# Optimization experiments

Hardware: AMD Instinct MI355X
Metric: run time of the kernel (lower is better)

Reference implementation:

```python
import jax, jax.numpy as jnp
import numpy as np

B = 128          # batch (number of ragged segments)
MAX_LEN = 197    # DeiT: 196 patches + CLS, upper bound on kept tokens
D = 768          # embed dim (DeiT-Base)
H = 12           # heads
HD = 64          # head dim
L = 6            # number of late ragged blocks
FF = 3072        # mlp hidden = 4*D
NC = 1000        # classes
EPS = 1e-6       # timm ViT LayerNorm eps


def setup_inputs() -> dict:
    # deterministic ragged lengths in [60, 197]; Total = 17078
    lens = 60 + (np.arange(B) * 137) % 138
    cu = np.concatenate([[0], np.cumsum(lens)]).astype(np.int32)
    total = int(cu[-1])
    ks = jax.random.split(jax.random.key(0), 8)
    n = lambda k, shp, s: jax.random.normal(k, shp, jnp.float32) * s
    return {
        "packed": n(ks[0], (total, D), 1.0),
        "cu_seqlens": jnp.asarray(cu),
        # stacked per-block params (jax convention: W is [in, out])
        "norm1_w": jnp.ones((L, D), jnp.float32),
        "norm1_b": jnp.zeros((L, D), jnp.float32),
        "qkv_w": n(ks[1], (L, D, 3 * D), 0.02),
        "qkv_b": jnp.zeros((L, 3 * D), jnp.float32),
        "proj_w": n(ks[2], (L, D, D), 0.02),
        "proj_b": jnp.zeros((L, D), jnp.float32),
        "norm2_w": jnp.ones((L, D), jnp.float32),
        "norm2_b": jnp.zeros((L, D), jnp.float32),
        "fc1_w": n(ks[3], (L, D, FF), 0.02),
        "fc1_b": jnp.zeros((L, FF), jnp.float32),
        "fc2_w": n(ks[4], (L, FF, D), 0.02),
        "fc2_b": jnp.zeros((L, D), jnp.float32),
        "backnorm_w": jnp.ones((D,), jnp.float32),
        "backnorm_b": jnp.zeros((D,), jnp.float32),
        "head_w": n(ks[5], (D, NC), 0.02),
        "head_b": jnp.zeros((NC,), jnp.float32),
    }


def _ln(x, w, b):
    mu = x.mean(-1, keepdims=True)
    var = ((x - mu) ** 2).mean(-1, keepdims=True)
    return (x - mu) * jax.lax.rsqrt(var + EPS) * w + b


def reference(packed, cu_seqlens, norm1_w, norm1_b, qkv_w, qkv_b, proj_w, proj_b,
              norm2_w, norm2_b, fc1_w, fc1_b, fc2_w, fc2_b,
              backnorm_w, backnorm_b, head_w, head_b):
    total = packed.shape[0]
    cu = cu_seqlens.astype(jnp.int32)
    b = cu.shape[0] - 1
    lens = cu[1:] - cu[:-1]                                   # [B]
    pos = jnp.arange(MAX_LEN, dtype=jnp.int32)
    idx = jnp.clip(cu[:-1, None] + pos[None, :], 0, total - 1)  # [B,S]
    valid = pos[None, :] < lens[:, None]                       # [B,S]
    # unpack ragged [Total,D] -> padded [B,S,D]; invalid slots zeroed
    x = packed[idx] * valid[..., None]
    kmask = valid[:, None, None, :]                            # [B,1,1,S] key mask
    scale = 1.0 / np.sqrt(HD)

    def block(x, p):
        n1w, n1b, qw, qb, pw, pb, n2w, n2b, f1w, f1b, f2w, f2b = p
        h = _ln(x, n1w, n1b)
        qkv = (h @ qw + qb).reshape(b, MAX_LEN, 3, H, HD)
        q, k, v = qkv[:, :, 0], qkv[:, :, 1], qkv[:, :, 2]
        sc = jnp.einsum('bqhd,bkhd->bhqk', q, k) * scale
        sc = jnp.where(kmask, sc, jnp.float32(-1e30))
        a = jax.nn.softmax(sc, axis=-1)
        o = jnp.einsum('bhqk,bkhd->bqhd', a, v).reshape(b, MAX_LEN, D)
        x = x + (o @ pw + pb)
        h2 = _ln(x, n2w, n2b)
        x = x + (jax.nn.gelu(h2 @ f1w + f1b, approximate=False) @ f2w + f2b)
        return x, None

    params = (norm1_w, norm1_b, qkv_w, qkv_b, proj_w, proj_b,
              norm2_w, norm2_b, fc1_w, fc1_b, fc2_w, fc2_b)
    x, _ = jax.lax.scan(block, x, params)
    # CLS token is the first token of each segment (packed[cu_seqlens[:-1]])
    cls = _ln(x[:, 0], backnorm_w, backnorm_b)
    return cls @ head_w + head_b
```

## Files before the change

kernel.cpp:

```cpp
#include <hip/hip_runtime.h>
#include <cstdint>
#include <cstddef>

typedef __bf16 bf16x8 __attribute__((ext_vector_type(8)));
typedef __bf16 bf16x4 __attribute__((ext_vector_type(4)));
typedef float  f32x4  __attribute__((ext_vector_type(4)));

#define M_TOT 17078
#define D_ 768
#define FF_ 3072
#define NC_ 1000
#define NL_ 6
#define PS 232

__device__ __forceinline__ void gload16(const __bf16* g, __bf16* s) {
    __builtin_amdgcn_global_load_lds(
        (const __attribute__((address_space(1))) unsigned int*)g,
        (__attribute__((address_space(3))) unsigned int*)s, 16, 0, 0);
}

__device__ __forceinline__ f32x4 mfma16(bf16x8 a, bf16x8 b, f32x4 c) {
    return __builtin_amdgcn_mfma_f32_16x16x32_bf16(a, b, c, 0, 0, 0);
}

__device__ __forceinline__ float fast_gelu(float v) {
    const float x = v * 0.70710678118654752440f;
    const float ax = fabsf(x);
    const float t = __builtin_amdgcn_rcpf(fmaf(0.3275911f, ax, 1.0f));
    float p = fmaf(1.061405429f, t, -1.453152027f);
    p = fmaf(p, t, 1.421413741f);
    p = fmaf(p, t, -0.284496736f);
    p = fmaf(p, t, 0.254829592f);
    const float e = __expf(-ax * ax);
    const float erf_ax = fmaf(-p * t, e, 1.0f);
    const float erf_x = copysignf(erf_ax, x);
    return 0.5f * v * (1.0f + erf_x);
}

__global__ __launch_bounds__(256)
void transpose_all_kernel(const float* __restrict__ qkvw, const float* __restrict__ projw,
                          const float* __restrict__ f1w, const float* __restrict__ f2w,
                          __bf16* __restrict__ qkvT, __bf16* __restrict__ projT,
                          __bf16* __restrict__ f1T, __bf16* __restrict__ f2T) {
    __shared__ float tile[32][33];
    int bid = blockIdx.x;
    const float* W; __bf16* WT; int N, local;
    if (bid < 1728)      { W = qkvw; WT = qkvT; N = 2304; local = bid; }
    else if (bid < 2304) { W = projw; WT = projT; N = 768; local = bid - 1728; }
    else if (bid < 4608) { W = f1w;  WT = f1T;  N = 3072; local = bid - 2304; }
    else                 { W = f2w;  WT = f2T;  N = 768;  local = bid - 4608; }
    const int nx = N >> 5;
    const int n0 = (local % nx) * 32, k0 = (local / nx) * 32;
    const int tc = threadIdx.x & 31, tr = threadIdx.x >> 5;
#pragma unroll
    for (int i = 0; i < 4; ++i)
        tile[tr + i * 8][tc] = W[(size_t)(k0 + tr + i * 8) * N + n0 + tc];
    __syncthreads();
    const int Kd = (bid < 4608) ? 768 : 3072;
#pragma unroll
    for (int i = 0; i < 4; ++i)
        WT[(size_t)(n0 + tr + i * 8) * Kd + k0 + tc] = (__bf16)tile[tc][tr + i * 8];
}

__global__ __launch_bounds__(256)
void transpose_head_kernel(const float* __restrict__ W, __bf16* __restrict__ WT) {
    __shared__ float tile[32][33];
    const int n0 = blockIdx.x * 32, k0 = blockIdx.y * 32;
    const int tc = threadIdx.x & 31, tr = threadIdx.x >> 5;
#pragma unroll
    for (int i = 0; i < 4; ++i) {
        const int n = n0 + tc;
        tile[tr + i * 8][tc] = (n < NC_) ? W[(size_t)(k0 + tr + i * 8) * NC_ + n] : 0.f;
    }
    __syncthreads();
#pragma unroll
    for (int i = 0; i < 4; ++i)
        WT[(size_t)(n0 + tr + i * 8) * 768 + k0 + tc] = (__bf16)tile[tc][tr + i * 8];
}

__global__ __launch_bounds__(256)
void ln_kernel(const float* __restrict__ X, const float* __restrict__ wgt,
               const float* __restrict__ bia, __bf16* __restrict__ out, int nrows) {
    const int wid = blockIdx.x * 4 + (threadIdx.x >> 6);
    if (wid >= nrows) return;
    const int l = threadIdx.x & 63;
    const float* xr = X + (size_t)wid * D_;
    f32x4 a[3];
#pragma unroll
    for (int i = 0; i < 3; ++i) a[i] = *(const f32x4*)(xr + i * 256 + l * 4);
    float s = 0.f, ss = 0.f;
#pragma unroll
    for (int i = 0; i < 3; ++i)
#pragma unroll
        for (int j = 0; j < 4; ++j) { float v = a[i][j]; s += v; ss += v * v; }
#pragma unroll
    for (int off = 32; off; off >>= 1) { s += __shfl_xor(s, off); ss += __shfl_xor(ss, off); }
    const float mean = s * (1.f / 768.f);
    const float var  = ss * (1.f / 768.f) - mean * mean;
    const float rstd = rsqrtf(var + 1e-6f);
#pragma unroll
    for (int i = 0; i < 3; ++i) {
        f32x4 wv = *(const f32x4*)(wgt + i * 256 + l * 4);
        f32x4 bv = *(const f32x4*)(bia + i * 256 + l * 4);
        bf16x4 ov;
#pragma unroll
        for (int j = 0; j < 4; ++j)
            ov[j] = (__bf16)((a[i][j] - mean) * rstd * wv[j] + bv[j]);
        *(bf16x4*)(out + (size_t)wid * D_ + i * 256 + l * 4) = ov;
    }
}

__global__ __launch_bounds__(256)
void cls_ln_kernel(const float* __restrict__ X, const int* __restrict__ cu,
                   const float* __restrict__ wgt, const float* __restrict__ bia,
                   __bf16* __restrict__ out) {
    const int wid = blockIdx.x * 4 + (threadIdx.x >> 6);
    const int l = threadIdx.x & 63;
    const float* xr = X + (size_t)cu[wid] * D_;
    f32x4 a[3];
#pragma unroll
    for (int i = 0; i < 3; ++i) a[i] = *(const f32x4*)(xr + i * 256 + l * 4);
    float s = 0.f, ss = 0.f;
#pragma unroll
    for (int i = 0; i < 3; ++i)
#pragma unroll
        for (int j = 0; j < 4; ++j) { float v = a[i][j]; s += v; ss += v * v; }
#pragma unroll
    for (int off = 32; off; off >>= 1) { s += __shfl_xor(s, off); ss += __shfl_xor(ss, off); }
    const float mean = s * (1.f / 768.f);
    const float var  = ss * (1.f / 768.f) - mean * mean;
    const float rstd = rsqrtf(var + 1e-6f);
#pragma unroll
    for (int i = 0; i < 3; ++i) {
        f32x4 wv = *(const f32x4*)(wgt + i * 256 + l * 4);
        f32x4 bv = *(const f32x4*)(bia + i * 256 + l * 4);
        bf16x4 ov;
#pragma unroll
        for (int j = 0; j < 4; ++j)
            ov[j] = (__bf16)((a[i][j] - mean) * rstd * wv[j] + bv[j]);
        *(bf16x4*)(out + (size_t)wid * D_ + i * 256 + l * 4) = ov;
    }
}

template <int EPI>
__global__ __launch_bounds__(256, 4)
void gemm_kernel(const __bf16* __restrict__ A, const __bf16* __restrict__ BT,
                 const float* __restrict__ bias, __bf16* __restrict__ Cb,
                 float* __restrict__ Cf, int K, int N, int Mc, int gx, int gy) {
    __shared__ __bf16 As[128 * 64];
    __shared__ __bf16 Bs[128 * 64];

    const int CC = 12;
    const int bid = blockIdx.x;
    const int per_chunk = gy * CC;
    const int chunk = bid / per_chunk;
    const int within = bid - chunk * per_chunk;
    const int ccw = min(CC, gx - chunk * CC);
    const int nb = gy * ccw;
    const int q = nb >> 3, r = nb & 7;
    const int xcd = within & 7, off = within >> 3;
    const int swz = (xcd < r) ? (xcd * (q + 1) + off) : (r * (q + 1) + (xcd - r) * q + off);
    const int by = swz / ccw;
    const int bx = chunk * CC + (swz - by * ccw);
    const int row0 = by * 128, col0 = bx * 128;

    const int t = threadIdx.x;
    const int l = t & 63, w = t >> 6;

    const int srow = t >> 3;
    const int scol = (((t & 7) ^ (srow & 7)) << 3);
    const __bf16* pa0 = A + (size_t)min(row0 +      srow, Mc - 1) * K + scol;
    const __bf16* pa1 = A + (size_t)min(row0 + 32 + srow, Mc - 1) * K + scol;
    const __bf16* pa2 = A + (size_t)min(row0 + 64 + srow, Mc - 1) * K + scol;
    const __bf16* pa3 = A + (size_t)min(row0 + 96 + srow, Mc - 1) * K + scol;
    const __bf16* pb0 = BT + (size_t)(col0 +      srow) * K + scol;
    const __bf16* pb1 = BT + (size_t)(col0 + 32 + srow) * K + scol;
    const __bf16* pb2 = BT + (size_t)(col0 + 64 + srow) * K + scol;
    const __bf16* pb3 = BT + (size_t)(col0 + 96 + srow) * K + scol;

    const int wr = (w >> 1) * 64, wc = (w & 1) * 64;
    const int fr = l & 15, fg = l >> 4;

    f32x4 acc[4][4];
#pragma unroll
    for (int i = 0; i < 4; ++i)
#pragma unroll
        for (int j = 0; j < 4; ++j) acc[i][j] = (f32x4){0.f, 0.f, 0.f, 0.f};

    for (int k0 = 0; k0 < K; k0 += 64) {
        __syncthreads();
        gload16(pa0 + k0, As + t * 8);
        gload16(pa1 + k0, As + 2048 + t * 8);
        gload16(pa2 + k0, As + 4096 + t * 8);
        gload16(pa3 + k0, As + 6144 + t * 8);
        gload16(pb0 + k0, Bs + t * 8);
        gload16(pb1 + k0, Bs + 2048 + t * 8);
        gload16(pb2 + k0, Bs + 4096 + t * 8);
        gload16(pb3 + k0, Bs + 6144 + t * 8);
        __syncthreads();
#pragma unroll
        for (int ks = 0; ks < 2; ++ks) {
            bf16x8 af[4], bfv[4];
#pragma unroll
            for (int i = 0; i < 4; ++i) {
                const int ar = wr + i * 16 + fr;
                const int br = wc + i * 16 + fr;
                af[i]  = *(const bf16x8*)(As + ar * 64 + (((ks * 4 + fg) ^ (ar & 7)) << 3));
                bfv[i] = *(const bf16x8*)(Bs + br * 64 + (((ks * 4 + fg) ^ (br & 7)) << 3));
            }
#pragma unroll
            for (int mi = 0; mi < 4; ++mi)
#pragma unroll
                for (int ni = 0; ni < 4; ++ni)
                    acc[mi][ni] = mfma16(af[mi], bfv[ni], acc[mi][ni]);
        }
    }

    if (EPI == 1) {
#pragma unroll
        for (int mi = 0; mi < 4; ++mi) {
#pragma unroll
            for (int ni = 0; ni < 4; ++ni) {
                const int nn = col0 + wc + ni * 16 + fr;
                const float bv = bias[nn];
#pragma unroll
                for (int v = 0; v < 4; ++v) {
                    const int mm = row0 + wr + mi * 16 + fg * 4 + v;
                    if (mm < Mc) {
                        float* p = Cf + (size_t)mm * N + nn;
                        *p = *p + acc[mi][ni][v] + bv;
                    }
                }
            }
        }
    } else {
        __syncthreads();
        __bf16* rs = As + w * 1024;
#pragma unroll
        for (int mi = 0; mi < 4; ++mi) {
#pragma unroll
            for (int ni = 0; ni < 4; ++ni) {
                const int nn = col0 + wc + ni * 16 + fr;
                const float bv = bias[nn];
#pragma unroll
                for (int v = 0; v < 4; ++v) {
                    const int row = fg * 4 + v;
                    float val = acc[mi][ni][v] + bv;
                    if (EPI == 2)
                        val = fast_gelu(val);
                    const int gsw = (ni * 2 + (fr >> 3)) ^ (row & 7);
                    rs[row * 64 + gsw * 8 + (fr & 7)] = (__bf16)val;
                }
            }
            asm volatile("s_waitcnt lgkmcnt(0)" ::: "memory");
#pragma unroll
            for (int half = 0; half < 2; ++half) {
                const int rr = (l >> 3) + half * 8;
                const int gg = (l & 7) ^ (rr & 7);
                bf16x8 vrow = *(const bf16x8*)(rs + rr * 64 + gg * 8);
                const int mm = row0 + wr + mi * 16 + rr;
                if (mm < Mc)
                    *(bf16x8*)(Cb + (size_t)mm * N + col0 + wc + (l & 7) * 8) = vrow;
            }
            asm volatile("s_waitcnt lgkmcnt(0)" ::: "memory");
        }
    }
}

__global__ __launch_bounds__(256)
void head_gemm_kernel(const __bf16* __restrict__ A, const __bf16* __restrict__ BT,
                      const float* __restrict__ bias, float* __restrict__ out) {
    __shared__ __bf16 As[128 * 32];
    __shared__ __bf16 Bs[128 * 32];
    const int t = threadIdx.x;
    const int l = t & 63, w = t >> 6;
    const int col0 = blockIdx.x * 128;
    const int sr = t >> 2, sc = (t & 3) * 8;
    const __bf16* a0 = A + (size_t)sr * 768 + sc;
    const __bf16* a1 = A + (size_t)(sr + 64) * 768 + sc;
    const __bf16* b0 = BT + (size_t)(col0 + sr) * 768 + sc;
    const __bf16* b1 = BT + (size_t)(col0 + sr + 64) * 768 + sc;
    __bf16* sa0 = As + t * 8;
    __bf16* sa1 = As + 2048 + t * 8;
    __bf16* sb0 = Bs + t * 8;
    __bf16* sb1 = Bs + 2048 + t * 8;
    const int wr = (w >> 1) * 64, wc = (w & 1) * 64;
    const int fr = l & 15, fg = l >> 4;

    f32x4 acc[4][4];
#pragma unroll
    for (int i = 0; i < 4; ++i)
#pragma unroll
        for (int j = 0; j < 4; ++j) acc[i][j] = (f32x4){0.f, 0.f, 0.f, 0.f};

    for (int k0 = 0; k0 < 768; k0 += 32) {
        __syncthreads();
        gload16(a0 + k0, sa0);
        gload16(a1 + k0, sa1);
        gload16(b0 + k0, sb0);
        gload16(b1 + k0, sb1);
        __syncthreads();
        bf16x8 af[4], bfv[4];
#pragma unroll
        for (int i = 0; i < 4; ++i) {
            af[i]  = *(const bf16x8*)(As + (wr + i * 16 + fr) * 32 + fg * 8);
            bfv[i] = *(const bf16x8*)(Bs + (wc + i * 16 + fr) * 32 + fg * 8);
        }
#pragma unroll
        for (int mi = 0; mi < 4; ++mi)
#pragma unroll
            for (int ni = 0; ni < 4; ++ni)
                acc[mi][ni] = mfma16(af[mi], bfv[ni], acc[mi][ni]);
    }

#pragma unroll
    for (int mi = 0; mi < 4; ++mi) {
#pragma unroll
        for (int ni = 0; ni < 4; ++ni) {
            const int nn = col0 + wc + ni * 16 + fr;
            if (nn < NC_) {
                const float bv = bias[nn];
#pragma unroll
                for (int v = 0; v < 4; ++v) {
                    const int mm = wr + mi * 16 + fg * 4 + v;
                    out[(size_t)mm * NC_ + nn] = acc[mi][ni][v] + bv;
                }
            }
        }
    }
}

__global__ __launch_bounds__(256)
void attn_kernel(const __bf16* __restrict__ qkv, __bf16* __restrict__ o,
                 const int* __restrict__ cu, int b0) {
    __shared__ __bf16 VT[64 * PS];
    __shared__ __bf16 P[4 * 16 * PS];
    const int b = b0 + blockIdx.x, h = blockIdx.y;
    const int r0   = cu[b0];
    const int rowb = cu[b] - r0;
    const int len  = cu[b + 1] - cu[b];
    const int t = threadIdx.x, w = t >> 6, l = t & 63;
    const int fr = l & 15, fg = l >> 4;
    const size_t base = (size_t)rowb * 2304 + h * 64;

    for (int c = t; c < 224 * 8; c += 256) {
        const int key = c >> 3, d0 = (c & 7) * 8;
        bf16x8 vv;
        if (key < len) {
            vv = *(const bf16x8*)(qkv + base + 1536 + (size_t)key * 2304 + d0);
        } else {
#pragma unroll
            for (int j = 0; j < 8; ++j) vv[j] = (__bf16)0.f;
        }
#pragma unroll
        for (int j = 0; j < 8; ++j) VT[(d0 + j) * PS + key] = vv[j];
    }
    __syncthreads();

    __bf16* Pw = P + w * 16 * PS;
    const int NQ = (len + 15) >> 4;

    for (int qt = w; qt < NQ; qt += 4) {
        const int qrow = qt * 16 + fr;
        const int qtok = qrow < len ? qrow : len - 1;
        const size_t qoff = base + (size_t)qtok * 2304 + fg * 8;
        bf16x8 qf0 = *(const bf16x8*)(qkv + qoff);
        bf16x8 qf1 = *(const bf16x8*)(qkv + qoff + 32);

        f32x4 s[14];
#pragma unroll
        for (int kt = 0; kt < 14; ++kt) {
            const int key = kt * 16 + fr;
            const int ktok = key < len ? key : len - 1;
            const size_t koff = base + 768 + (size_t)ktok * 2304 + fg * 8;
            f32x4 a = {0.f, 0.f, 0.f, 0.f};
            a = mfma16(qf0, *(const bf16x8*)(qkv + koff), a);
            a = mfma16(qf1, *(const bf16x8*)(qkv + koff + 32), a);
            s[kt] = a;
        }

#pragma unroll
        for (int v = 0; v < 4; ++v) {
            float m = -1e30f;
#pragma unroll
            for (int kt = 0; kt < 14; ++kt) {
                float sv = (kt * 16 + fr < len) ? s[kt][v] * 0.125f : -1e30f;
                s[kt][v] = sv;
                m = fmaxf(m, sv);
            }
            m = fmaxf(m, __shfl_xor(m, 1, 16));
            m = fmaxf(m, __shfl_xor(m, 2, 16));
            m = fmaxf(m, __shfl_xor(m, 4, 16));
            m = fmaxf(m, __shfl_xor(m, 8, 16));
            float sum = 0.f;
#pragma unroll
            for (int kt = 0; kt < 14; ++kt) {
                float p = __expf(s[kt][v] - m);
                s[kt][v] = p;
                sum += p;
            }
            sum += __shfl_xor(sum, 1, 16);
            sum += __shfl_xor(sum, 2, 16);
            sum += __shfl_xor(sum, 4, 16);
            sum += __shfl_xor(sum, 8, 16);
            const float inv = 1.f / sum;
#pragma unroll
            for (int kt = 0; kt < 14; ++kt)
                Pw[(fg * 4 + v) * PS + kt * 16 + fr] = (__bf16)(s[kt][v] * inv);
        }
        asm volatile("s_waitcnt lgkmcnt(0)" ::: "memory");

#pragma unroll
        for (int nt = 0; nt < 4; ++nt) {
            f32x4 oa = {0.f, 0.f, 0.f, 0.f};
#pragma unroll
            for (int ks = 0; ks < 7; ++ks) {
                bf16x8 pa = *(const bf16x8*)(Pw + fr * PS + ks * 32 + fg * 8);
                bf16x8 vb = *(const bf16x8*)(VT + (nt * 16 + fr) * PS + ks * 32 + fg * 8);
                oa = mfma16(pa, vb, oa);
            }
#pragma unroll
            for (int v = 0; v < 4; ++v) {
                const int q = qt * 16 + fg * 4 + v;
                if (q < len)
                    o[(size_t)(rowb + q) * D_ + h * 64 + nt * 16 + fr] = (__bf16)oa[v];
            }
        }
    }
}

extern "C" void kernel_launch(void* const* d_in, const int* in_sizes, int n_in,
                              void* d_out, int out_size, void* d_ws, size_t ws_size,
                              hipStream_t stream) {
    const float* packed = (const float*)d_in[0];
    const int*   cu     = (const int*)d_in[1];
    const float* n1w = (const float*)d_in[2];
    const float* n1b = (const float*)d_in[3];
    const float* qkvw = (const float*)d_in[4];
    const float* qkvb = (const float*)d_in[5];
    const float* projw = (const float*)d_in[6];
    const float* projb = (const float*)d_in[7];
    const float* n2w = (const float*)d_in[8];
    const float* n2b = (const float*)d_in[9];
    const float* f1w = (const float*)d_in[10];
    const float* f1b = (const float*)d_in[11];
    const float* f2w = (const float*)d_in[12];
    const float* f2b = (const float*)d_in[13];
    const float* bnw = (const float*)d_in[14];
    const float* bnb = (const float*)d_in[15];
    const float* hw  = (const float*)d_in[16];
    const float* hb  = (const float*)d_in[17];
    float* out = (float*)d_out;
    (void)in_sizes; (void)n_in; (void)out_size;

    int cuh[129];
    cuh[0] = 0;
    for (int i = 0; i < 128; ++i) cuh[i + 1] = cuh[i] + 60 + (i * 137) % 138;

    const size_t SZ_X    = (size_t)M_TOT * D_ * 4;
    const size_t SZ_H    = (size_t)M_TOT * D_ * 2;
    const size_t SZ_W    = (size_t)(2304 * 768 + 768 * 768 + 768 * 3072 + 3072 * 768) * 2;
    const size_t OB_FULL = (size_t)M_TOT * D_ * 2;
    const size_t OB_SMALL= (size_t)5702 * D_ * 2;
    const size_t CB_XL   = (size_t)M_TOT * FF_ * 2;
    const size_t CB_L    = (size_t)M_TOT * 2304 * 2;
    const size_t CB_S    = (size_t)5702 * 2304 * 2;
    const size_t need_XL = SZ_X + SZ_H + OB_FULL + SZ_W + CB_XL;
    const size_t need_L  = SZ_X + SZ_H + OB_FULL + SZ_W + CB_L;

    int nq, nf; size_t cb_bytes, ob_bytes;
    if (ws_size >= need_XL)     { nq = 1; nf = 1; cb_bytes = CB_XL; ob_bytes = OB_FULL; }
    else if (ws_size >= need_L) { nq = 1; nf = 2; cb_bytes = CB_L;  ob_bytes = OB_FULL; }
    else                        { nq = 4; nf = 4; cb_bytes = CB_S;  ob_bytes = OB_SMALL; }

    char* ws = (char*)d_ws;
    float*  x        = (float*)ws;   ws += SZ_X;
    __bf16* hbuf     = (__bf16*)ws;  ws += SZ_H;
    __bf16* obuf     = (__bf16*)ws;  ws += ob_bytes;
    __bf16* qkvT     = (__bf16*)ws;  ws += (size_t)2304 * 768 * 2;
    __bf16* projT    = (__bf16*)ws;  ws += (size_t)768 * 768 * 2;
    __bf16* f1T      = (__bf16*)ws;  ws += (size_t)768 * 3072 * 2;
    __bf16* f2T      = (__bf16*)ws;  ws += (size_t)3072 * 768 * 2;
    __bf16* chunkbuf = (__bf16*)ws;  ws += cb_bytes;
    __bf16* clsb   = chunkbuf;
    __bf16* headWT = chunkbuf + (size_t)128 * 768;

    hipMemcpyAsync(x, packed, SZ_X, hipMemcpyDeviceToDevice, stream);

    const int lngrid = (M_TOT + 3) / 4;
    const int frows = (M_TOT + nf - 1) / nf;

    for (int L = 0; L < NL_; ++L) {
        transpose_all_kernel<<<6912, 256, 0, stream>>>(
            qkvw + (size_t)L * 768 * 2304, projw + (size_t)L * 768 * 768,
            f1w + (size_t)L * 768 * 3072, f2w + (size_t)L * 3072 * 768,
            qkvT, projT, f1T, f2T);

        ln_kernel<<<lngrid, 256, 0, stream>>>(x, n1w + L * 768, n1b + L * 768, hbuf, M_TOT);
        for (int c = 0; c < nq; ++c) {
            const int b0c = c * (128 / nq);
            const int bcnt = 128 / nq;
            const int R0 = cuh[b0c];
            const int Mc = cuh[b0c + bcnt] - R0;
            const int gy = (Mc + 127) / 128;
            gemm_kernel<0><<<18 * gy, 256, 0, stream>>>(
                hbuf + (size_t)R0 * D_, qkvT, qkvb + (size_t)L * 2304, chunkbuf, nullptr, 768, 2304, Mc, 18, gy);
            attn_kernel<<<dim3(bcnt, 12), 256, 0, stream>>>(chunkbuf, obuf, cu, b0c);
            gemm_kernel<1><<<6 * gy, 256, 0, stream>>>(
                obuf, projT, projb + (size_t)L * 768, nullptr, x + (size_t)R0 * D_, 768, 768, Mc, 6, gy);
        }
        ln_kernel<<<lngrid, 256, 0, stream>>>(x, n2w + L * 768, n2b + L * 768, hbuf, M_TOT);
        for (int c = 0; c < nf; ++c) {
            const int r0 = c * frows;
            const int Mc = (M_TOT - r0) < frows ? (M_TOT - r0) : frows;
            const int gy = (Mc + 127) / 128;
            gemm_kernel<2><<<24 * gy, 256, 0, stream>>>(
                hbuf + (size_t)r0 * D_, f1T, f1b + (size_t)L * 3072, chunkbuf, nullptr, 768, 3072, Mc, 24, gy);
            gemm_kernel<1><<<6 * gy, 256, 0, stream>>>(
                chunkbuf, f2T, f2b + (size_t)L * 768, nullptr, x + (size_t)r0 * D_, 3072, 768, Mc, 6, gy);
        }
    }
    cls_ln_kernel<<<32, 256, 0, stream>>>(x, cu, bnw, bnb, clsb);
    transpose_head_kernel<<<dim3(32, 24), 256, 0, stream>>>(hw, headWT);
    head_gemm_kernel<<<8, 256, 0, stream>>>(clsb, headWT, hb, out);
}
```

Baseline: 2.568 ms.

## Store residual stream in bf16 and use staged vectorized residual epilogue

The fp32 residual buffer x becomes bf16. The initial memcpy is replaced by a conversion kernel, and the LayerNorm kernels now read bf16. The residual-add GEMM epilogue now goes through the same LDS-staged, 16-byte vectorized path as the other epilogues, doing a read-modify-write in bf16 instead of scattered scalar fp32 updates. This halves residual traffic and coalesces the stores, at the cost of accumulating the residual stream in bf16, which may hurt accuracy over the six blocks.

```diff
diff --git a/kernel.cpp b/kernel.cpp
--- a/kernel.cpp
+++ b/kernel.cpp
@@ -35,6 +35,18 @@
     const float erf_ax = fmaf(-p * t, e, 1.0f);
     const float erf_x = copysignf(erf_ax, x);
     return 0.5f * v * (1.0f + erf_x);
+}
+
+__global__ __launch_bounds__(256)
+void convert_x_kernel(const float* __restrict__ in, __bf16* __restrict__ out, int n4) {
+    const int i = blockIdx.x * 256 + threadIdx.x;
+    if (i < n4) {
+        f32x4 v = *(const f32x4*)(in + (size_t)i * 4);
+        bf16x4 o;
+#pragma unroll
+        for (int j = 0; j < 4; ++j) o[j] = (__bf16)v[j];
+        *(bf16x4*)(out + (size_t)i * 4) = o;
+    }
 }
 
 __global__ __launch_bounds__(256)
@@ -79,15 +91,19 @@
 }
 
 __global__ __launch_bounds__(256)
-void ln_kernel(const float* __restrict__ X, const float* __restrict__ wgt,
+void ln_kernel(const __bf16* __restrict__ X, const float* __restrict__ wgt,
                const float* __restrict__ bia, __bf16* __restrict__ out, int nrows) {
     const int wid = blockIdx.x * 4 + (threadIdx.x >> 6);
     if (wid >= nrows) return;
     const int l = threadIdx.x & 63;
-    const float* xr = X + (size_t)wid * D_;
+    const __bf16* xr = X + (size_t)wid * D_;
     f32x4 a[3];
 #pragma unroll
-    for (int i = 0; i < 3; ++i) a[i] = *(const f32x4*)(xr + i * 256 + l * 4);
+    for (int i = 0; i < 3; ++i) {
+        bf16x4 t = *(const bf16x4*)(xr + i * 256 + l * 4);
+#pragma unroll
+        for (int j = 0; j < 4; ++j) a[i][j] = (float)t[j];
+    }
     float s = 0.f, ss = 0.f;
 #pragma unroll
     for (int i = 0; i < 3; ++i)
@@ -111,15 +127,19 @@
 }
 
 __global__ __launch_bounds__(256)
-void cls_ln_kernel(const float* __restrict__ X, const int* __restrict__ cu,
+void cls_ln_kernel(const __bf16* __restrict__ X, const int* __restrict__ cu,
                    const float* __restrict__ wgt, const float* __restrict__ bia,
                    __bf16* __restrict__ out) {
     const int wid = blockIdx.x * 4 + (threadIdx.x >> 6);
     const int l = threadIdx.x & 63;
-    const float* xr = X + (size_t)cu[wid] * D_;
+    const __bf16* xr = X + (size_t)cu[wid] * D_;
     f32x4 a[3];
 #pragma unroll
-    for (int i = 0; i < 3; ++i) a[i] = *(const f32x4*)(xr + i * 256 + l * 4);
+    for (int i = 0; i < 3; ++i) {
+        bf16x4 t = *(const bf16x4*)(xr + i * 256 + l * 4);
+#pragma unroll
+        for (int j = 0; j < 4; ++j) a[i][j] = (float)t[j];
+    }
     float s = 0.f, ss = 0.f;
 #pragma unroll
     for (int i = 0; i < 3; ++i)
@@ -146,7 +166,7 @@
 __global__ __launch_bounds__(256, 4)
 void gemm_kernel(const __bf16* __restrict__ A, const __bf16* __restrict__ BT,
                  const float* __restrict__ bias, __bf16* __restrict__ Cb,
-                 float* __restrict__ Cf, int K, int N, int Mc, int gx, int gy) {
+                 int K, int N, int Mc, int gx, int gy) {
     __shared__ __bf16 As[128 * 64];
     __shared__ __bf16 Bs[128 * 64];
 
@@ -216,54 +236,43 @@
         }
     }
 
-    if (EPI == 1) {
-#pragma unroll
-        for (int mi = 0; mi < 4; ++mi) {
-#pragma unroll
-            for (int ni = 0; ni < 4; ++ni) {
-                const int nn = col0 + wc + ni * 16 + fr;
-                const float bv = bias[nn];
-#pragma unroll
-                for (int v = 0; v < 4; ++v) {
-                    const int mm = row0 + wr + mi * 16 + fg * 4 + v;
-                    if (mm < Mc) {
-                        float* p = Cf + (size_t)mm * N + nn;
-                        *p = *p + acc[mi][ni][v] + bv;
-                    }
+    __syncthreads();
+    __bf16* rs = As + w * 1024;
+#pragma unroll
+    for (int mi = 0; mi < 4; ++mi) {
+#pragma unroll
+        for (int ni = 0; ni < 4; ++ni) {
+            const int nn = col0 + wc + ni * 16 + fr;
+            const float bv = bias[nn];
+#pragma unroll
+            for (int v = 0; v < 4; ++v) {
+                const int row = fg * 4 + v;
+                float val = acc[mi][ni][v] + bv;
+                if (EPI == 2)
+                    val = fast_gelu(val);
+                const int gsw = (ni * 2 + (fr >> 3)) ^ (row & 7);
+                rs[row * 64 + gsw * 8 + (fr & 7)] = (__bf16)val;
+            }
+        }
+        asm volatile("s_waitcnt lgkmcnt(0)" ::: "memory");
+#pragma unroll
+        for (int half = 0; half < 2; ++half) {
+            const int rr = (l >> 3) + half * 8;
+            const int gg = (l & 7) ^ (rr & 7);
+            bf16x8 vrow = *(const bf16x8*)(rs + rr * 64 + gg * 8);
+            const int mm = row0 + wr + mi * 16 + rr;
+            if (mm < Mc) {
+                __bf16* pc = Cb + (size_t)mm * N + col0 + wc + (l & 7) * 8;
+                if (EPI == 1) {
+                    bf16x8 xold = *(const bf16x8*)pc;
+#pragma unroll
+                    for (int j = 0; j < 8; ++j)
+                        vrow[j] = (__bf16)((float)xold[j] + (float)vrow[j]);
                 }
-            }
-        }
-    } else {
-        __syncthreads();
-        __bf16* rs = As + w * 1024;
-#pragma unroll
-        for (int mi = 0; mi < 4; ++mi) {
-#pragma unroll
-            for (int ni = 0; ni < 4; ++ni) {
-                const int nn = col0 + wc + ni * 16 + fr;
-                const float bv = bias[nn];
-#pragma unroll
-                for (int v = 0; v < 4; ++v) {
-                    const int row = fg * 4 + v;
-                    float val = acc[mi][ni][v] + bv;
-                    if (EPI == 2)
-                        val = fast_gelu(val);
-                    const int gsw = (ni * 2 + (fr >> 3)) ^ (row & 7);
-                    rs[row * 64 + gsw * 8 + (fr & 7)] = (__bf16)val;
-                }
-            }
-            asm volatile("s_waitcnt lgkmcnt(0)" ::: "memory");
-#pragma unroll
-            for (int half = 0; half < 2; ++half) {
-                const int rr = (l >> 3) + half * 8;
-                const int gg = (l & 7) ^ (rr & 7);
-                bf16x8 vrow = *(const bf16x8*)(rs + rr * 64 + gg * 8);
-                const int mm = row0 + wr + mi * 16 + rr;
-                if (mm < Mc)
-                    *(bf16x8*)(Cb + (size_t)mm * N + col0 + wc + (l & 7) * 8) = vrow;
-            }
-            asm volatile("s_waitcnt lgkmcnt(0)" ::: "memory");
-        }
+                *(bf16x8*)pc = vrow;
+            }
+        }
+        asm volatile("s_waitcnt lgkmcnt(0)" ::: "memory");
     }
 }
 
@@ -457,7 +466,7 @@
     cuh[0] = 0;
     for (int i = 0; i < 128; ++i) cuh[i + 1] = cuh[i] + 60 + (i * 137) % 138;
 
-    const size_t SZ_X    = (size_t)M_TOT * D_ * 4;
+    const size_t SZ_X    = (size_t)M_TOT * D_ * 2;
     const size_t SZ_H    = (size_t)M_TOT * D_ * 2;
     const size_t SZ_W    = (size_t)(2304 * 768 + 768 * 768 + 768 * 3072 + 3072 * 768) * 2;
     const size_t OB_FULL = (size_t)M_TOT * D_ * 2;
@@ -474,7 +483,7 @@
     else                        { nq = 4; nf = 4; cb_bytes = CB_S;  ob_bytes = OB_SMALL; }
 
     char* ws = (char*)d_ws;
-    float*  x        = (float*)ws;   ws += SZ_X;
+    __bf16* x        = (__bf16*)ws;  ws += SZ_X;
     __bf16* hbuf     = (__bf16*)ws;  ws += SZ_H;
     __bf16* obuf     = (__bf16*)ws;  ws += ob_bytes;
     __bf16* qkvT     = (__bf16*)ws;  ws += (size_t)2304 * 768 * 2;
@@ -485,7 +494,8 @@
     __bf16* clsb   = chunkbuf;
     __bf16* headWT = chunkbuf + (size_t)128 * 768;
 
-    hipMemcpyAsync(x, packed, SZ_X, hipMemcpyDeviceToDevice, stream);
+    const int n4 = M_TOT * D_ / 4;
+    convert_x_kernel<<<(n4 + 255) / 256, 256, 0, stream>>>(packed, x, n4);
 
     const int lngrid = (M_TOT + 3) / 4;
     const int frows = (M_TOT + nf - 1) / nf;
@@ -504,10 +514,10 @@
             const int Mc = cuh[b0c + bcnt] - R0;
             const int gy = (Mc + 127) / 128;
             gemm_kernel<0><<<18 * gy, 256, 0, stream>>>(
-                hbuf + (size_t)R0 * D_, qkvT, qkvb + (size_t)L * 2304, chunkbuf, nullptr, 768, 2304, Mc, 18, gy);
+                hbuf + (size_t)R0 * D_, qkvT, qkvb + (size_t)L * 2304, chunkbuf, 768, 2304, Mc, 18, gy);
             attn_kernel<<<dim3(bcnt, 12), 256, 0, stream>>>(chunkbuf, obuf, cu, b0c);
             gemm_kernel<1><<<6 * gy, 256, 0, stream>>>(
-                obuf, projT, projb + (size_t)L * 768, nullptr, x + (size_t)R0 * D_, 768, 768, Mc, 6, gy);
+                obuf, projT, projb + (size_t)L * 768, x + (size_t)R0 * D_, 768, 768, Mc, 6, gy);
         }
         ln_kernel<<<lngrid, 256, 0, stream>>>(x, n2w + L * 768, n2b + L * 768, hbuf, M_TOT);
         for (int c = 0; c < nf; ++c) {
@@ -515,9 +525,9 @@
             const int Mc = (M_TOT - r0) < frows ? (M_TOT - r0) : frows;
             const int gy = (Mc + 127) / 128;
             gemm_kernel<2><<<24 * gy, 256, 0, stream>>>(
-                hbuf + (size_t)r0 * D_, f1T, f1b + (size_t)L * 3072, chunkbuf, nullptr, 768, 3072, Mc, 24, gy);
+                hbuf + (size_t)r0 * D_, f1T, f1b + (size_t)L * 3072, chunkbuf, 768, 3072, Mc, 24, gy);
             gemm_kernel<1><<<6 * gy, 256, 0, stream>>>(
-                chunkbuf, f2T, f2b + (size_t)L * 768, nullptr, x + (size_t)r0 * D_, 3072, 768, Mc, 6, gy);
+                chunkbuf, f2T, f2b + (size_t)L * 768, x + (size_t)r0 * D_, 3072, 768, Mc, 6, gy);
         }
     }
     cls_ln_kernel<<<32, 256, 0, stream>>>(x, cu, bnw, bnb, clsb);
```

Result: faster. 2.389 ms (-7.0%).
